# Optimization experiments

Measured on AMD Instinct MI355X. Metric: run time of the kernel, lower is better.

The kernel has to match this reference:

```python
import jax, jax.numpy as jnp
import numpy as np

L = 2; B = 16; H = 56; W = 56; N = H * W; D = 256
HEADS = 8; HD = 32; INNER = HEADS * HD
WIN = 7; WIN2 = WIN * WIN; NWH = H // WIN; NWW = W // WIN; NW = NWH * NWW
DISP = WIN // 2; FF = 4 * D; CPB = 512; EPS = 1e-5


def _shift_masks():
    d = DISP
    ul = np.zeros((WIN2, WIN2), np.float32)
    ul[-d * WIN:, :-d * WIN] = -np.inf
    ul[:-d * WIN, -d * WIN:] = -np.inf
    lr = np.zeros((WIN, WIN, WIN, WIN), np.float32)
    lr[:, -d:, :, :-d] = -np.inf
    lr[:, :-d, :, -d:] = -np.inf
    return jnp.asarray(ul), jnp.asarray(lr.reshape(WIN2, WIN2))

MASK_UL, MASK_LR = _shift_masks()

_idx = np.array([[i, j] for i in range(WIN) for j in range(WIN)], np.float32)
_rel = _idx[None, :, :] - _idx[:, None, :]  # (49,49,2) relative distances
REL = jnp.asarray((np.sign(_rel) * np.log1p(np.abs(_rel))).reshape(WIN2 * WIN2, 2))


def _ln(x, g, b):
    m = x.mean(-1, keepdims=True)
    v = ((x - m) ** 2).mean(-1, keepdims=True)
    return (x - m) / jnp.sqrt(v + EPS) * g + b


def _l2norm(t):
    return t / jnp.maximum(jnp.linalg.norm(t, axis=-1, keepdims=True), 1e-12)


def _window_attn(xm, qkv_w, tau, cw1, cb1, cw2, cb2, ow, ob, shifted):
    if shifted:
        xm = jnp.roll(xm, (-DISP, -DISP), (1, 2))
    qkv = xm @ qkv_w  # (B,H,W,3*INNER), no bias
    q, k, v = jnp.split(qkv, 3, axis=-1)

    def towin(t):  # (B,H,W,INNER) -> (B,heads,nw,win2,hd)
        t = t.reshape(B, NWH, WIN, NWW, WIN, HEADS, HD)
        return t.transpose(0, 5, 1, 3, 2, 4, 6).reshape(B, HEADS, NW, WIN2, HD)

    q, k, v = towin(q), towin(k), towin(v)
    # cosine-similarity attention
    dots = jnp.einsum('bhwid,bhwjd->bhwij', _l2norm(q), _l2norm(k))
    dots = dots / jnp.clip(tau, 0.01, None)[None, :, None, None, None]
    # continuous position bias MLP: 2 -> CPB -> heads
    cpb = (jax.nn.relu(REL @ cw1 + cb1) @ cw2 + cb2).reshape(WIN2, WIN2, HEADS)
    dots = dots + cpb.transpose(2, 0, 1)[None, :, None]
    if shifted:
        dots = dots.at[:, :, -NWW:].add(MASK_UL)
        dots = dots.at[:, :, NWW - 1::NWW].add(MASK_LR)
    attn = jax.nn.softmax(dots, -1)
    out = jnp.einsum('bhwij,bhwjd->bhwid', attn, v)
    out = out.reshape(B, HEADS, NWH, NWW, WIN, WIN, HD)
    out = out.transpose(0, 2, 4, 3, 5, 1, 6).reshape(B, H, W, INNER)
    out = out @ ow + ob
    if shifted:
        out = jnp.roll(out, (DISP, DISP), (1, 2))
    return out


def _forward(x, spe, qkv_w, tau, cw1, cb1, cw2, cb2, ow, ob, ln1_g, ln1_b,
             fw1, fb1, fw2, fb2, ln2_g, ln2_b, norm_g, norm_b):
    xm = (x + spe).reshape(B, H, W, D)
    for i in range(L):
        shifted = (i % 2 == 1)
        a = _window_attn(xm, qkv_w[i], tau[i], cw1[i], cb1[i], cw2[i], cb2[i],
                         ow[i], ob[i], shifted)
        xm = _ln(a, ln1_g[i], ln1_b[i]) + xm  # Residual(PostNorm(attn))
        f = jax.nn.gelu(xm @ fw1[i] + fb1[i], approximate=False) @ fw2[i] + fb2[i]
        xm = _ln(f, ln2_g[i], ln2_b[i]) + xm  # Residual(PostNorm(mlp))
    return _ln(xm, norm_g, norm_b).reshape(B, N, D)


def setup_inputs():
    key = jax.random.key(0)
    ks = jax.random.split(key, 10)
    rn = lambda k, shp, s: jax.random.normal(k, shp, jnp.float32) * s
    return {
        'x': rn(ks[0], (B, N, D), 1.0),
        'spatial_position_embedding': rn(ks[1], (B, N, D), 0.02),
        'qkv_w': rn(ks[2], (L, D, 3 * INNER), 0.02),
        'tau': jnp.ones((L, HEADS), jnp.float32),
        'cw1': rn(ks[3], (L, 2, CPB), 0.1),
        'cb1': jnp.zeros((L, CPB), jnp.float32),
        'cw2': rn(ks[4], (L, CPB, HEADS), 0.05),
        'cb2': jnp.zeros((L, HEADS), jnp.float32),
        'ow': rn(ks[5], (L, INNER, D), 0.02),
        'ob': jnp.zeros((L, D), jnp.float32),
        'ln1_g': jnp.ones((L, D), jnp.float32),
        'ln1_b': jnp.zeros((L, D), jnp.float32),
        'fw1': rn(ks[6], (L, D, FF), 0.02),
        'fb1': jnp.zeros((L, FF), jnp.float32),
        'fw2': rn(ks[7], (L, FF, D), 0.02),
        'fb2': jnp.zeros((L, D), jnp.float32),
        'ln2_g': jnp.ones((L, D), jnp.float32),
        'ln2_b': jnp.zeros((L, D), jnp.float32),
        'norm_g': jnp.ones((D,), jnp.float32),
        'norm_b': jnp.zeros((D,), jnp.float32),
    }


def reference(x, spatial_position_embedding, qkv_w, tau, cw1, cb1, cw2, cb2, ow, ob,
              ln1_g, ln1_b, fw1, fb1, fw2, fb2, ln2_g, ln2_b, norm_g, norm_b):
    return _forward(x, spatial_position_embedding, qkv_w, tau, cw1, cb1, cw2, cb2,
                    ow, ob, ln1_g, ln1_b, fw1, fb1, fw2, fb2, ln2_g, ln2_b,
                    norm_g, norm_b)
```

## Files before the change

### kernel.cpp

```cpp
#include <hip/hip_runtime.h>
#include <hip/hip_bf16.h>
#include <math.h>

typedef short    short8  __attribute__((ext_vector_type(8)));
typedef float    floatx4 __attribute__((ext_vector_type(4)));

__device__ __forceinline__ float b2f(unsigned short u) {
    union { float f; unsigned int i; } v; v.i = ((unsigned int)u) << 16; return v.f;
}
__device__ __forceinline__ unsigned short f2b(float f) {
    union { float f; unsigned int i; } v; v.f = f;
    unsigned int b = v.i;
    return (unsigned short)((b + 0x7FFFu + ((b >> 16) & 1u)) >> 16);
}
__device__ __forceinline__ float rd(const void* p, long i, int f) {
    return f ? ((const float*)p)[i] : b2f(((const unsigned short*)p)[i]);
}
__device__ __forceinline__ float fgelu(float x) {
    float x2 = x * x;
    float t = x * fmaf(x2, -0.0713548163f, -1.5957691216f);
    return __fdividef(x, 1.f + __expf(t));
}
__device__ __forceinline__ int xcd_swz(int bid, int nwg) {
    int q = nwg >> 3, r = nwg & 7;
    int xcd = bid & 7, loc = bid >> 3;
    return ((xcd < r) ? xcd * (q + 1) : r * (q + 1) + (xcd - r) * q) + loc;
}

#define NTOK_ 50176

__global__ __launch_bounds__(256) void k_detect(const unsigned short* __restrict__ x,
                                                int* __restrict__ flag) {
    __shared__ int cnt;
    if (threadIdx.x == 0) cnt = 0;
    __syncthreads();
    unsigned short v = x[threadIdx.x];
    int e = (v >> 7) & 0xFF;
    if (e >= 0x90) atomicAdd(&cnt, 1);
    __syncthreads();
    if (threadIdx.x == 0) *flag = (cnt >= 8) ? 1 : 0;
}

__global__ __launch_bounds__(256) void k_add_spe(const void* __restrict__ x,
                                                 const void* __restrict__ spe,
                                                 float* __restrict__ xm,
                                                 unsigned short* __restrict__ xb,
                                                 const int* __restrict__ flagp) {
    const int f = *flagp;
    long i = ((long)blockIdx.x * 256 + threadIdx.x) * 4;
    float4 o;
    if (f) {
        float4 a = *(const float4*)((const float*)x + i);
        float4 b = *(const float4*)((const float*)spe + i);
        o.x = a.x + b.x; o.y = a.y + b.y; o.z = a.z + b.z; o.w = a.w + b.w;
    } else {
        ushort4 a = *(const ushort4*)((const unsigned short*)x + i);
        ushort4 b = *(const ushort4*)((const unsigned short*)spe + i);
        o.x = b2f(a.x) + b2f(b.x); o.y = b2f(a.y) + b2f(b.y);
        o.z = b2f(a.z) + b2f(b.z); o.w = b2f(a.w) + b2f(b.w);
    }
    *(float4*)(xm + i) = o;
    if (xb) {
        ushort4 h; h.x = f2b(o.x); h.y = f2b(o.y); h.z = f2b(o.z); h.w = f2b(o.w);
        *(ushort4*)(xb + i) = h;
    }
}

__global__ __launch_bounds__(256) void k_transpose(const void* __restrict__ in, long ioff,
                                                   unsigned short* __restrict__ out,
                                                   int K, int N,
                                                   const int* __restrict__ flagp) {
    __shared__ unsigned short tile[32][33];
    const int f = *flagp;
    int n0 = blockIdx.x * 32, k0 = blockIdx.y * 32;
    int tx = threadIdx.x & 31, ty = threadIdx.x >> 5;
#pragma unroll
    for (int i = 0; i < 4; i++) {
        int k = k0 + ty + i * 8;
        long idx = ioff + (long)k * N + n0 + tx;
        unsigned short v = f ? f2b(((const float*)in)[idx])
                             : ((const unsigned short*)in)[idx];
        tile[ty + i * 8][tx] = v;
    }
    __syncthreads();
#pragma unroll
    for (int i = 0; i < 4; i++) {
        int n = n0 + ty + i * 8;
        out[(long)n * K + k0 + tx] = tile[tx][ty + i * 8];
    }
}

__global__ __launch_bounds__(512) void k_cpb(const void* __restrict__ cw1,
                                             const void* __restrict__ cb1,
                                             const void* __restrict__ cw2,
                                             const void* __restrict__ cb2,
                                             float* __restrict__ cpb,
                                             const int* __restrict__ flagp) {
    const int f = *flagp;
    int p = blockIdx.x;
    int l = blockIdx.y;
    int t = threadIdx.x;
    int i = p / 49, j = p - i * 49;
    int yi = i / 7, xi = i - yi * 7, yj = j / 7, xj = j - yj * 7;
    float dy = (float)(yj - yi), dx = (float)(xj - xi);
    float sy = (dy > 0.f) ? 1.f : ((dy < 0.f) ? -1.f : 0.f);
    float sx = (dx > 0.f) ? 1.f : ((dx < 0.f) ? -1.f : 0.f);
    float r0 = sy * log1pf(fabsf(dy));
    float r1 = sx * log1pf(fabsf(dx));
    float h = r0 * rd(cw1, l * 1024 + t, f) + r1 * rd(cw1, l * 1024 + 512 + t, f)
            + rd(cb1, l * 512 + t, f);
    h = fmaxf(h, 0.f);
    __shared__ float red[512];
    for (int hh = 0; hh < 8; hh++) {
        red[t] = h * rd(cw2, (long)(l * 512 + t) * 8 + hh, f);
        __syncthreads();
        for (int s = 256; s > 0; s >>= 1) {
            if (t < s) red[t] += red[t + s];
            __syncthreads();
        }
        if (t == 0) cpb[((long)l * 8 + hh) * 2401 + p] = red[0] + rd(cb2, l * 8 + hh, f);
        __syncthreads();
    }
}

__global__ __launch_bounds__(256) void k_cast_roll(const float* __restrict__ xmg,
                                                   unsigned short* __restrict__ xb, int shift) {
    int gid = blockIdx.x * 256 + threadIdx.x;
    int c4 = (gid & 63) * 4;
    int t = gid >> 6;
    int x = t % 56; int t2 = t / 56;
    int y = t2 % 56;
    int b = t2 / 56;
    int ys = y + shift; if (ys >= 56) ys -= 56;
    int xs = x + shift; if (xs >= 56) xs -= 56;
    float4 v = *(const float4*)(xmg + (((long)b * 3136 + ys * 56 + xs) * 256 + c4));
    ushort4 o; o.x = f2b(v.x); o.y = f2b(v.y); o.z = f2b(v.z); o.w = f2b(v.w);
    *(ushort4*)(xb + ((long)t * 256 + c4)) = o;
}

__global__ __launch_bounds__(256) void gemm_bt(const unsigned short* __restrict__ A,
                                               const unsigned short* __restrict__ Bt,
                                               const void* __restrict__ bias, long boff,
                                               void* __restrict__ Cp,
                                               int M, int N, int K, int flags,
                                               const int* __restrict__ flagp) {
    __shared__ __align__(16) unsigned short smem[16896];
    unsigned short* As = smem;
    const int f = *flagp;
    const int tid = threadIdx.x;
    const int lane = tid & 63;
    const int wave = tid >> 6;
    const int wrow = (wave >> 1) * 64;
    const int wcol = (wave & 1) * 64;

    const int nwg = gridDim.x * gridDim.y;
    const int nb = xcd_swz(blockIdx.y * gridDim.x + blockIdx.x, nwg);
    const int bn = nb % gridDim.x, bm = nb / gridDim.x;

    floatx4 acc[4][4] = {};

    const int arow = tid >> 2;
    const int aseg = (tid & 3) * 8;
    const unsigned short* Ag = A + (long)(bm * 128 + arow) * K + aseg;
    const long rstep = (long)64 * K;

    const int q = lane >> 4;
    const int mrow = lane & 15;

    const unsigned short* Brow[4];
#pragma unroll
    for (int nt = 0; nt < 4; nt++)
        Brow[nt] = Bt + (long)(bn * 128 + wcol + nt * 16 + mrow) * K + q * 8;

    uint4 a_cur0 = *(const uint4*)(Ag);
    uint4 a_cur1 = *(const uint4*)(Ag + rstep);
    short8 bf_cur[4], bf_nxt[4];
#pragma unroll
    for (int nt = 0; nt < 4; nt++) bf_cur[nt] = *(const short8*)(Brow[nt]);

    for (int k0 = 0; k0 < K; k0 += 32) {
        const int kn = k0 + 32;
        uint4 a_nxt0, a_nxt1;
        if (kn < K) {
            a_nxt0 = *(const uint4*)(Ag + kn);
            a_nxt1 = *(const uint4*)(Ag + kn + rstep);
#pragma unroll
            for (int nt = 0; nt < 4; nt++) bf_nxt[nt] = *(const short8*)(Brow[nt] + kn);
        }
        __syncthreads();
        *(uint4*)(As + arow * 40 + aseg) = a_cur0;
        *(uint4*)(As + (arow + 64) * 40 + aseg) = a_cur1;
        __syncthreads();

        short8 af_[4];
#pragma unroll
        for (int mt = 0; mt < 4; mt++)
            af_[mt] = *(const short8*)(As + (wrow + mt * 16 + mrow) * 40 + q * 8);
#pragma unroll
        for (int mt = 0; mt < 4; mt++)
#pragma unroll
            for (int nt = 0; nt < 4; nt++)
                acc[mt][nt] = __builtin_amdgcn_mfma_f32_16x16x32_bf16(af_[mt], bf_cur[nt], acc[mt][nt], 0, 0, 0);
        if (kn < K) {
            a_cur0 = a_nxt0; a_cur1 = a_nxt1;
#pragma unroll
            for (int nt = 0; nt < 4; nt++) bf_cur[nt] = bf_nxt[nt];
        }
    }

    __syncthreads();

    unsigned short* T = smem;
#pragma unroll
    for (int nt = 0; nt < 4; nt++) {
        int col = wcol + nt * 16 + mrow;
        float bv = (flags & 1) ? rd(bias, boff + bn * 128 + col, f) : 0.f;
#pragma unroll
        for (int mt = 0; mt < 4; mt++) {
            int row0 = wrow + mt * 16 + q * 4;
#pragma unroll
            for (int r = 0; r < 4; r++) {
                float v = acc[mt][nt][r] + bv;
                if (flags & 2) v = fgelu(v);
                T[(row0 + r) * 132 + col] = f2b(v);
            }
        }
    }
    __syncthreads();
    unsigned short* Cu = (unsigned short*)Cp;
    int row = tid >> 4;
    int col8 = (tid & 15) * 8;
#pragma unroll
    for (int p = 0; p < 8; p++) {
        int rr = p * 16 + row;
        *(uint4*)(Cu + (long)(bm * 128 + rr) * N + bn * 128 + col8) =
            *(const uint4*)(T + rr * 132 + col8);
    }
}

__global__ __launch_bounds__(256) void gemm_ln(const unsigned short* __restrict__ A,
                                               const unsigned short* __restrict__ Bt,
                                               const void* __restrict__ bias, long boff,
                                               const void* __restrict__ g, long goff,
                                               const void* __restrict__ bb, long b2off,
                                               float* __restrict__ xm,
                                               unsigned short* __restrict__ xb,
                                               int K, int xbmode,
                                               const int* __restrict__ flagp) {
    __shared__ __align__(16) unsigned short smem[17152];
    __shared__ float pp[4][32][2];
    unsigned short* As = smem;
    const int f = *flagp;
    const int tid = threadIdx.x;
    const int lane = tid & 63;
    const int wv = tid >> 6;
    const int wcol = wv * 64;
    const int bm = blockIdx.x;

    floatx4 acc[2][4] = {};
    const int brow = tid >> 2;
    const int bseg = (tid & 3) * 8;
    const unsigned short* Ag = A + (long)(bm * 32 + brow) * K + bseg;
    const int q = lane >> 4;
    const int c = lane & 15;

    const unsigned short* Brow[4];
#pragma unroll
    for (int nt = 0; nt < 4; nt++)
        Brow[nt] = Bt + (long)(wcol + nt * 16 + c) * K + q * 8;

    uint4 a_cur;
    if (tid < 128) a_cur = *(const uint4*)(Ag);
    short8 bf_cur[4], bf_nxt[4];
#pragma unroll
    for (int nt = 0; nt < 4; nt++) bf_cur[nt] = *(const short8*)(Brow[nt]);

    for (int k0 = 0; k0 < K; k0 += 32) {
        const int kn = k0 + 32;
        uint4 a_nxt;
        if (kn < K) {
            if (tid < 128) a_nxt = *(const uint4*)(Ag + kn);
#pragma unroll
            for (int nt = 0; nt < 4; nt++) bf_nxt[nt] = *(const short8*)(Brow[nt] + kn);
        }
        __syncthreads();
        if (tid < 128) *(uint4*)(As + brow * 40 + bseg) = a_cur;
        __syncthreads();

        short8 af_[2];
#pragma unroll
        for (int mt = 0; mt < 2; mt++)
            af_[mt] = *(const short8*)(As + (mt * 16 + c) * 40 + q * 8);
#pragma unroll
        for (int mt = 0; mt < 2; mt++)
#pragma unroll
            for (int nt = 0; nt < 4; nt++)
                acc[mt][nt] = __builtin_amdgcn_mfma_f32_16x16x32_bf16(af_[mt], bf_cur[nt], acc[mt][nt], 0, 0, 0);
        if (kn < K) {
            if (tid < 128) a_cur = a_nxt;
#pragma unroll
            for (int nt = 0; nt < 4; nt++) bf_cur[nt] = bf_nxt[nt];
        }
    }
    __syncthreads();

    float bv[4];
#pragma unroll
    for (int nt = 0; nt < 4; nt++)
        bv[nt] = rd(bias, boff + wcol + nt * 16 + c, f);
#pragma unroll
    for (int mt = 0; mt < 2; mt++) {
#pragma unroll
        for (int r = 0; r < 4; r++) {
            float s1 = 0.f, s2 = 0.f;
#pragma unroll
            for (int nt = 0; nt < 4; nt++) {
                float v = acc[mt][nt][r] + bv[nt];
                s1 += v; s2 += v * v;
            }
            s1 += __shfl_xor(s1, 1); s2 += __shfl_xor(s2, 1);
            s1 += __shfl_xor(s1, 2); s2 += __shfl_xor(s2, 2);
            s1 += __shfl_xor(s1, 4); s2 += __shfl_xor(s2, 4);
            s1 += __shfl_xor(s1, 8); s2 += __shfl_xor(s2, 8);
            if (c == 0) {
                pp[wv][mt * 16 + q * 4 + r][0] = s1;
                pp[wv][mt * 16 + q * 4 + r][1] = s2;
            }
        }
    }

    const int c0 = lane * 4;
    float4 gv, bbv;
    gv.x = rd(g, goff + c0 + 0, f); gv.y = rd(g, goff + c0 + 1, f);
    gv.z = rd(g, goff + c0 + 2, f); gv.w = rd(g, goff + c0 + 3, f);
    bbv.x = rd(bb, b2off + c0 + 0, f); bbv.y = rd(bb, b2off + c0 + 1, f);
    bbv.z = rd(bb, b2off + c0 + 2, f); bbv.w = rd(bb, b2off + c0 + 3, f);

    float* Tf = (float*)smem;
#pragma unroll
    for (int mt = 0; mt < 2; mt++)
#pragma unroll
        for (int nt = 0; nt < 4; nt++)
#pragma unroll
            for (int r = 0; r < 4; r++)
                Tf[(mt * 16 + q * 4 + r) * 268 + wcol + nt * 16 + c] = acc[mt][nt][r] + bv[nt];
    __syncthreads();
#pragma unroll
    for (int it = 0; it < 8; it++) {
        int row = wv * 8 + it;
        float sum = pp[0][row][0] + pp[1][row][0] + pp[2][row][0] + pp[3][row][0];
        float ssq = pp[0][row][1] + pp[1][row][1] + pp[2][row][1] + pp[3][row][1];
        float mean = sum * (1.f / 256.f);
        float var = ssq * (1.f / 256.f) - mean * mean;
        float rstd = rsqrtf(fmaxf(var, 0.f) + 1e-5f);
        long tok = (long)(bm * 32 + row);
        long grow = tok * 256;
        float4 t = *(const float4*)(Tf + row * 268 + c0);
        float4 xv = *(const float4*)(xm + grow + c0);
        float4 o;
        o.x = (t.x - mean) * rstd * gv.x + bbv.x + xv.x;
        o.y = (t.y - mean) * rstd * gv.y + bbv.y + xv.y;
        o.z = (t.z - mean) * rstd * gv.z + bbv.z + xv.z;
        o.w = (t.w - mean) * rstd * gv.w + bbv.w + xv.w;
        *(float4*)(xm + grow + c0) = o;
        if (xbmode) {
            long xg = grow;
            if (xbmode == 2) {
                int bi = (int)(tok / 3136); int r2 = (int)(tok - (long)bi * 3136);
                int y = r2 / 56; int x = r2 - y * 56;
                y = (y >= 3) ? y - 3 : y + 53;
                x = (x >= 3) ? x - 3 : x + 53;
                xg = ((long)bi * 3136 + y * 56 + x) * 256;
            }
            ushort4 hb; hb.x = f2b(o.x); hb.y = f2b(o.y); hb.z = f2b(o.z); hb.w = f2b(o.w);
            *(ushort4*)(xb + xg + c0) = hb;
        }
    }
}

__global__ __launch_bounds__(256) void k_attn(const unsigned short* __restrict__ qkv,
                                              const float* __restrict__ cpb,
                                              const void* __restrict__ tau, long toff,
                                              unsigned short* __restrict__ out,
                                              int shifted,
                                              const int* __restrict__ flagp) {
    __shared__ __align__(16) unsigned short Pbuf[4][64 * 72];
    __shared__ __align__(16) unsigned short Vt[4][32 * 72];
    __shared__ float inq_s[4][64], ink_s[4][64];

    const int f = *flagp;
    const int tid = threadIdx.x;
    const int wv = tid >> 6;
    const int lane = tid & 63;
    const int h = blockIdx.x * 4 + wv;
    const int w = blockIdx.y, b = blockIdx.z;
    const int wy = w >> 3, wx = w & 7;
    const int q = lane >> 4;
    const int c = lane & 15;

    short8 qa[4], kb[4];
    float sqv[4], skv[4];
#pragma unroll
    for (int mt = 0; mt < 4; mt++) {
        int i = mt * 16 + c; if (i > 48) i = 48;
        int py = i / 7, px = i - py * 7;
        long base = (((long)b * 56 + wy * 7 + py) * 56 + wx * 7 + px) * 768 + h * 32 + q * 8;
        qa[mt] = *(const short8*)(qkv + base);
        kb[mt] = *(const short8*)(qkv + base + 256);
        float sq = 0.f, sk = 0.f;
#pragma unroll
        for (int e = 0; e < 8; e++) {
            float a = b2f((unsigned short)qa[mt][e]); sq += a * a;
            float k2 = b2f((unsigned short)kb[mt][e]); sk += k2 * k2;
        }
        sqv[mt] = sq; skv[mt] = sk;
    }
#pragma unroll
    for (int mt = 0; mt < 4; mt++) {
        float sq = sqv[mt]; sq += __shfl_xor(sq, 16); sq += __shfl_xor(sq, 32);
        float sk = skv[mt]; sk += __shfl_xor(sk, 16); sk += __shfl_xor(sk, 32);
        if (q == 0) {
            inq_s[wv][mt * 16 + c] = 1.f / fmaxf(sqrtf(sq), 1e-12f);
            ink_s[wv][mt * 16 + c] = 1.f / fmaxf(sqrtf(sk), 1e-12f);
        }
    }

    floatx4 acc[4][4] = {};
#pragma unroll
    for (int mt = 0; mt < 4; mt++)
#pragma unroll
        for (int nt = 0; nt < 4; nt++)
            acc[mt][nt] = __builtin_amdgcn_mfma_f32_16x16x32_bf16(qa[mt], kb[nt], acc[mt][nt], 0, 0, 0);

#pragma unroll
    for (int z = lane; z < 576; z += 64)
        *(uint2*)(&Vt[wv][z * 4]) = make_uint2(0u, 0u);
    if (lane < 49) {
        int py = lane / 7, px = lane - py * 7;
        long base = (((long)b * 56 + wy * 7 + py) * 56 + wx * 7 + px) * 768 + h * 32 + 512;
#pragma unroll
        for (int dd = 0; dd < 32; dd += 8) {
            ushort4 v0 = *(const ushort4*)(qkv + base + dd);
            ushort4 v1 = *(const ushort4*)(qkv + base + dd + 4);
            Vt[wv][(dd + 0) * 72 + lane] = v0.x;
            Vt[wv][(dd + 1) * 72 + lane] = v0.y;
            Vt[wv][(dd + 2) * 72 + lane] = v0.z;
            Vt[wv][(dd + 3) * 72 + lane] = v0.w;
            Vt[wv][(dd + 4) * 72 + lane] = v1.x;
            Vt[wv][(dd + 5) * 72 + lane] = v1.y;
            Vt[wv][(dd + 6) * 72 + lane] = v1.z;
            Vt[wv][(dd + 7) * 72 + lane] = v1.w;
        }
    }

    float scale = 1.f / fmaxf(rd(tau, toff + h, f), 0.01f);
#pragma unroll
    for (int mt = 0; mt < 4; mt++) {
#pragma unroll
        for (int r = 0; r < 4; r++) {
            int i = mt * 16 + q * 4 + r;
            int ci = (i < 49) ? i : 48;
            int pyi = ci / 7, pxi = ci - pyi * 7;
            float qi = inq_s[wv][ci] * scale;
            float vals[4];
#pragma unroll
            for (int nt = 0; nt < 4; nt++) {
                int j = nt * 16 + c;
                if (j < 49) {
                    float v = acc[mt][nt][r] * qi * ink_s[wv][j]
                            + cpb[h * 2401 + ci * 49 + j];
                    if (shifted) {
                        int pyj = j / 7, pxj = j - pyj * 7;
                        if (wy == 7 && ((pyi >= 4) != (pyj >= 4))) v = -1e30f;
                        if (wx == 7 && ((pxi >= 4) != (pxj >= 4))) v = -1e30f;
                    }
                    vals[nt] = v;
                } else vals[nt] = -1e30f;
            }
            float m = fmaxf(fmaxf(vals[0], vals[1]), fmaxf(vals[2], vals[3]));
            m = fmaxf(m, __shfl_xor(m, 1)); m = fmaxf(m, __shfl_xor(m, 2));
            m = fmaxf(m, __shfl_xor(m, 4)); m = fmaxf(m, __shfl_xor(m, 8));
            float s = 0.f;
#pragma unroll
            for (int nt = 0; nt < 4; nt++) { vals[nt] = __expf(vals[nt] - m); s += vals[nt]; }
            s += __shfl_xor(s, 1); s += __shfl_xor(s, 2);
            s += __shfl_xor(s, 4); s += __shfl_xor(s, 8);
            float rinv = 1.f / s;
#pragma unroll
            for (int nt = 0; nt < 4; nt++)
                Pbuf[wv][i * 72 + nt * 16 + c] = f2b(vals[nt] * rinv);
        }
    }

    floatx4 accO[4][2] = {};
#pragma unroll
    for (int ks = 0; ks < 2; ks++) {
        short8 pa[4], vb[2];
#pragma unroll
        for (int mt = 0; mt < 4; mt++)
            pa[mt] = *(const short8*)(&Pbuf[wv][(mt * 16 + c) * 72 + ks * 32 + q * 8]);
#pragma unroll
        for (int nt = 0; nt < 2; nt++)
            vb[nt] = *(const short8*)(&Vt[wv][(nt * 16 + c) * 72 + ks * 32 + q * 8]);
#pragma unroll
        for (int mt = 0; mt < 4; mt++)
#pragma unroll
            for (int nt = 0; nt < 2; nt++)
                accO[mt][nt] = __builtin_amdgcn_mfma_f32_16x16x32_bf16(pa[mt], vb[nt], accO[mt][nt], 0, 0, 0);
    }

    int sh = shifted ? 3 : 0;
#pragma unroll
    for (int mt = 0; mt < 4; mt++) {
#pragma unroll
        for (int r = 0; r < 4; r++) {
            int i = mt * 16 + q * 4 + r;
            if (i < 49) {
                int py = i / 7, px = i - py * 7;
                int yo = wy * 7 + py + sh; if (yo >= 56) yo -= 56;
                int xo = wx * 7 + px + sh; if (xo >= 56) xo -= 56;
                long ob = (((long)b * 56 + yo) * 56 + xo) * 256 + h * 32;
                out[ob + c]      = f2b(accO[mt][0][r]);
                out[ob + 16 + c] = f2b(accO[mt][1][r]);
            }
        }
    }
}

__global__ __launch_bounds__(256) void k_final(const float* __restrict__ xm,
                                               const void* __restrict__ g,
                                               const void* __restrict__ bb,
                                               void* __restrict__ out,
                                               const int* __restrict__ flagp) {
    const int f = *flagp;
    int t = blockIdx.x, c = threadIdx.x;
    long off = (long)t * 256 + c;
    float v = xm[off];
    __shared__ float red[256];
    red[c] = v; __syncthreads();
#pragma unroll
    for (int s = 128; s > 0; s >>= 1) {
        if (c < s) red[c] += red[c + s];
        __syncthreads();
    }
    float mean = red[0] * (1.f / 256.f);
    __syncthreads();
    float d = v - mean;
    red[c] = d * d; __syncthreads();
#pragma unroll
    for (int s = 128; s > 0; s >>= 1) {
        if (c < s) red[c] += red[c + s];
        __syncthreads();
    }
    float var = red[0] * (1.f / 256.f);
    float ln = d * rsqrtf(var + 1e-5f) * rd(g, c, f) + rd(bb, c, f);
    if (f) ((float*)out)[off] = ln;
    else   ((unsigned short*)out)[off] = f2b(ln);
}

extern "C" void kernel_launch(void* const* d_in, const int* in_sizes, int n_in,
                              void* d_out, int out_size, void* d_ws, size_t ws_size,
                              hipStream_t stream) {
    char* ws = (char*)d_ws;
    float*          xm    = (float*)(ws + 0);
    unsigned short* wt    = (unsigned short*)(ws + 51380224);
    float*          cpb   = (float*)(ws + 54525952);
    int*            flagp = (int*)(ws + 54679616);
    const size_t DYN = 54680576;

    long Mg = NTOK_; int G = 1;
    while (G <= 8) {
        Mg = NTOK_ / G;
        if (DYN + (size_t)Mg * 2560 <= ws_size) break;
        G <<= 1;
    }
    if (G > 8) { G = 8; Mg = NTOK_ / 8; }
    const int NB = 16 / G;
    const bool fused = (G == 1);

    unsigned short* xb   = (unsigned short*)(ws + DYN);
    unsigned short* qkvb = (unsigned short*)(ws + DYN + Mg * 512);
    unsigned short* hid  = (unsigned short*)(ws + DYN + Mg * 512);

    k_detect<<<1, 256, 0, stream>>>((const unsigned short*)d_in[0], flagp);

    for (int l = 0; l < 2; l++) {
        unsigned short* base = wt + (long)l * 786432;
        k_transpose<<<dim3(24, 8), 256, 0, stream>>>(d_in[2],  (long)l * 196608, base,          256, 768,  flagp);
        k_transpose<<<dim3(8, 8),  256, 0, stream>>>(d_in[8],  (long)l * 65536,  base + 196608, 256, 256,  flagp);
        k_transpose<<<dim3(32, 8), 256, 0, stream>>>(d_in[12], (long)l * 262144, base + 262144, 256, 1024, flagp);
        k_transpose<<<dim3(8, 32), 256, 0, stream>>>(d_in[14], (long)l * 262144, base + 524288, 1024, 256, flagp);
    }
    k_cpb<<<dim3(2401, 2), 512, 0, stream>>>(d_in[4], d_in[5], d_in[6], d_in[7], cpb, flagp);
    k_add_spe<<<dim3(12544), 256, 0, stream>>>(d_in[0], d_in[1], xm,
                                               fused ? xb : (unsigned short*)nullptr, flagp);

    for (int l = 0; l < 2; l++) {
        int sh = (l & 1) ? 3 : 0;
        unsigned short* base = wt + (long)l * 786432;
        for (int g = 0; g < G; g++) {
            long m0 = (long)g * Mg;
            if (!fused)
                k_cast_roll<<<dim3(Mg / 4), 256, 0, stream>>>(xm + m0 * 256, xb, sh);
            gemm_bt<<<dim3(6, Mg / 128), 256, 0, stream>>>(xb, base, nullptr, 0, qkvb,
                                                           (int)Mg, 768, 256, 4, flagp);
            k_attn<<<dim3(2, 64, NB), 256, 0, stream>>>(qkvb, cpb + (long)l * 19208,
                                                        d_in[3], (long)l * 8, xb, (l & 1), flagp);
            gemm_ln<<<dim3(Mg / 32), 256, 0, stream>>>(xb, base + 196608, d_in[9], (long)l * 256,
                                                       d_in[10], (long)l * 256, d_in[11], (long)l * 256,
                                                       xm + m0 * 256, xb, 256, 1, flagp);
            gemm_bt<<<dim3(8, Mg / 128), 256, 0, stream>>>(xb, base + 262144, d_in[13], (long)l * 1024,
                                                           hid, (int)Mg, 1024, 256, 1 | 2 | 4, flagp);
            int xbm = fused ? ((l == 0) ? 2 : 0) : 1;
            gemm_ln<<<dim3(Mg / 32), 256, 0, stream>>>(hid, base + 524288, d_in[15], (long)l * 256,
                                                       d_in[16], (long)l * 256, d_in[17], (long)l * 256,
                                                       xm + m0 * 256, xb, 1024, xbm, flagp);
        }
    }
    k_final<<<dim3(NTOK_), 256, 0, stream>>>(xm, d_in[18], d_in[19], d_out, flagp);
}
```

Measured before the change: 1.027 ms.

## Stage B tiles through LDS in gemm_ln and fuse final LayerNorm into last layer

The gemm_ln kernel now loads the weight (B) tile cooperatively into shared memory each K step, replacing per-wave direct global register loads with register double-buffering. This cuts redundant global loads of B but drops the software prefetch. In the fused path, the last layer's FFN gemm_ln also applies the final LayerNorm and writes straight to the output, skipping k_final and the xm writeback. Skipping that writeback assumes xm is not needed afterwards.

```diff
diff --git a/kernel.cpp b/kernel.cpp
--- a/kernel.cpp
+++ b/kernel.cpp
@@ -246,10 +246,14 @@
                                                float* __restrict__ xm,
                                                unsigned short* __restrict__ xb,
                                                int K, int xbmode,
+                                               const void* __restrict__ fg,
+                                               const void* __restrict__ fb,
+                                               void* __restrict__ outp,
                                                const int* __restrict__ flagp) {
     __shared__ __align__(16) unsigned short smem[17152];
     __shared__ float pp[4][32][2];
     unsigned short* As = smem;
+    unsigned short* Bs = smem + 1280;
     const int f = *flagp;
     const int tid = threadIdx.x;
     const int lane = tid & 63;
@@ -261,46 +265,38 @@
     const int brow = tid >> 2;
     const int bseg = (tid & 3) * 8;
     const unsigned short* Ag = A + (long)(bm * 32 + brow) * K + bseg;
+    const unsigned short* Bg = Bt + (long)brow * K + bseg;
+    const long brow2 = (long)64 * K;
     const int q = lane >> 4;
     const int c = lane & 15;
 
-    const unsigned short* Brow[4];
-#pragma unroll
-    for (int nt = 0; nt < 4; nt++)
-        Brow[nt] = Bt + (long)(wcol + nt * 16 + c) * K + q * 8;
-
-    uint4 a_cur;
-    if (tid < 128) a_cur = *(const uint4*)(Ag);
-    short8 bf_cur[4], bf_nxt[4];
-#pragma unroll
-    for (int nt = 0; nt < 4; nt++) bf_cur[nt] = *(const short8*)(Brow[nt]);
-
     for (int k0 = 0; k0 < K; k0 += 32) {
-        const int kn = k0 + 32;
-        uint4 a_nxt;
-        if (kn < K) {
-            if (tid < 128) a_nxt = *(const uint4*)(Ag + kn);
-#pragma unroll
-            for (int nt = 0; nt < 4; nt++) bf_nxt[nt] = *(const short8*)(Brow[nt] + kn);
-        }
-        __syncthreads();
-        if (tid < 128) *(uint4*)(As + brow * 40 + bseg) = a_cur;
-        __syncthreads();
-
-        short8 af_[2];
+        uint4 a0;
+        if (tid < 128) a0 = *(const uint4*)(Ag + k0);
+        uint4 b0 = *(const uint4*)(Bg + k0);
+        uint4 b1 = *(const uint4*)(Bg + k0 + brow2);
+        uint4 b2 = *(const uint4*)(Bg + k0 + 2 * brow2);
+        uint4 b3 = *(const uint4*)(Bg + k0 + 3 * brow2);
+        __syncthreads();
+        if (tid < 128) *(uint4*)(As + brow * 40 + bseg) = a0;
+        *(uint4*)(Bs + brow * 40 + bseg) = b0;
+        *(uint4*)(Bs + (brow + 64) * 40 + bseg) = b1;
+        *(uint4*)(Bs + (brow + 128) * 40 + bseg) = b2;
+        *(uint4*)(Bs + (brow + 192) * 40 + bseg) = b3;
+        __syncthreads();
+
+        short8 af_[2], bf_[4];
 #pragma unroll
         for (int mt = 0; mt < 2; mt++)
             af_[mt] = *(const short8*)(As + (mt * 16 + c) * 40 + q * 8);
 #pragma unroll
+        for (int nt = 0; nt < 4; nt++)
+            bf_[nt] = *(const short8*)(Bs + (wcol + nt * 16 + c) * 40 + q * 8);
+#pragma unroll
         for (int mt = 0; mt < 2; mt++)
 #pragma unroll
             for (int nt = 0; nt < 4; nt++)
-                acc[mt][nt] = __builtin_amdgcn_mfma_f32_16x16x32_bf16(af_[mt], bf_cur[nt], acc[mt][nt], 0, 0, 0);
-        if (kn < K) {
-            if (tid < 128) a_cur = a_nxt;
-#pragma unroll
-            for (int nt = 0; nt < 4; nt++) bf_cur[nt] = bf_nxt[nt];
-        }
+                acc[mt][nt] = __builtin_amdgcn_mfma_f32_16x16x32_bf16(af_[mt], bf_[nt], acc[mt][nt], 0, 0, 0);
     }
     __syncthreads();
 
@@ -330,11 +326,17 @@
     }
 
     const int c0 = lane * 4;
-    float4 gv, bbv;
+    float4 gv, bbv, fgv, fbv;
     gv.x = rd(g, goff + c0 + 0, f); gv.y = rd(g, goff + c0 + 1, f);
     gv.z = rd(g, goff + c0 + 2, f); gv.w = rd(g, goff + c0 + 3, f);
     bbv.x = rd(bb, b2off + c0 + 0, f); bbv.y = rd(bb, b2off + c0 + 1, f);
     bbv.z = rd(bb, b2off + c0 + 2, f); bbv.w = rd(bb, b2off + c0 + 3, f);
+    if (xbmode == 3) {
+        fgv.x = rd(fg, c0 + 0, f); fgv.y = rd(fg, c0 + 1, f);
+        fgv.z = rd(fg, c0 + 2, f); fgv.w = rd(fg, c0 + 3, f);
+        fbv.x = rd(fb, c0 + 0, f); fbv.y = rd(fb, c0 + 1, f);
+        fbv.z = rd(fb, c0 + 2, f); fbv.w = rd(fb, c0 + 3, f);
+    }
 
     float* Tf = (float*)smem;
 #pragma unroll
@@ -362,18 +364,43 @@
         o.y = (t.y - mean) * rstd * gv.y + bbv.y + xv.y;
         o.z = (t.z - mean) * rstd * gv.z + bbv.z + xv.z;
         o.w = (t.w - mean) * rstd * gv.w + bbv.w + xv.w;
-        *(float4*)(xm + grow + c0) = o;
-        if (xbmode) {
-            long xg = grow;
-            if (xbmode == 2) {
-                int bi = (int)(tok / 3136); int r2 = (int)(tok - (long)bi * 3136);
-                int y = r2 / 56; int x = r2 - y * 56;
-                y = (y >= 3) ? y - 3 : y + 53;
-                x = (x >= 3) ? x - 3 : x + 53;
-                xg = ((long)bi * 3136 + y * 56 + x) * 256;
+        if (xbmode == 3) {
+            float s1 = o.x + o.y + o.z + o.w;
+            s1 += __shfl_xor(s1, 1); s1 += __shfl_xor(s1, 2);
+            s1 += __shfl_xor(s1, 4); s1 += __shfl_xor(s1, 8);
+            s1 += __shfl_xor(s1, 16); s1 += __shfl_xor(s1, 32);
+            float fmean = s1 * (1.f / 256.f);
+            float d0 = o.x - fmean, d1 = o.y - fmean, d2 = o.z - fmean, d3 = o.w - fmean;
+            float s2 = d0 * d0 + d1 * d1 + d2 * d2 + d3 * d3;
+            s2 += __shfl_xor(s2, 1); s2 += __shfl_xor(s2, 2);
+            s2 += __shfl_xor(s2, 4); s2 += __shfl_xor(s2, 8);
+            s2 += __shfl_xor(s2, 16); s2 += __shfl_xor(s2, 32);
+            float frstd = rsqrtf(s2 * (1.f / 256.f) + 1e-5f);
+            float r0 = d0 * frstd * fgv.x + fbv.x;
+            float r1 = d1 * frstd * fgv.y + fbv.y;
+            float r2 = d2 * frstd * fgv.z + fbv.z;
+            float r3 = d3 * frstd * fgv.w + fbv.w;
+            if (f) {
+                float4 fo; fo.x = r0; fo.y = r1; fo.z = r2; fo.w = r3;
+                *(float4*)((float*)outp + grow + c0) = fo;
+            } else {
+                ushort4 ho; ho.x = f2b(r0); ho.y = f2b(r1); ho.z = f2b(r2); ho.w = f2b(r3);
+                *(ushort4*)((unsigned short*)outp + grow + c0) = ho;
             }
-            ushort4 hb; hb.x = f2b(o.x); hb.y = f2b(o.y); hb.z = f2b(o.z); hb.w = f2b(o.w);
-            *(ushort4*)(xb + xg + c0) = hb;
+        } else {
+            *(float4*)(xm + grow + c0) = o;
+            if (xbmode) {
+                long xg = grow;
+                if (xbmode == 2) {
+                    int bi = (int)(tok / 3136); int r2i = (int)(tok - (long)bi * 3136);
+                    int y = r2i / 56; int x = r2i - y * 56;
+                    y = (y >= 3) ? y - 3 : y + 53;
+                    x = (x >= 3) ? x - 3 : x + 53;
+                    xg = ((long)bi * 3136 + y * 56 + x) * 256;
+                }
+                ushort4 hb; hb.x = f2b(o.x); hb.y = f2b(o.y); hb.z = f2b(o.z); hb.w = f2b(o.w);
+                *(ushort4*)(xb + xg + c0) = hb;
+            }
         }
     }
 }
@@ -608,14 +635,17 @@
                                                         d_in[3], (long)l * 8, xb, (l & 1), flagp);
             gemm_ln<<<dim3(Mg / 32), 256, 0, stream>>>(xb, base + 196608, d_in[9], (long)l * 256,
                                                        d_in[10], (long)l * 256, d_in[11], (long)l * 256,
-                                                       xm + m0 * 256, xb, 256, 1, flagp);
+                                                       xm + m0 * 256, xb, 256, 1,
+                                                       d_in[18], d_in[19], d_out, flagp);
             gemm_bt<<<dim3(8, Mg / 128), 256, 0, stream>>>(xb, base + 262144, d_in[13], (long)l * 1024,
                                                            hid, (int)Mg, 1024, 256, 1 | 2 | 4, flagp);
-            int xbm = fused ? ((l == 0) ? 2 : 0) : 1;
+            int xbm = fused ? ((l == 0) ? 2 : 3) : 1;
             gemm_ln<<<dim3(Mg / 32), 256, 0, stream>>>(hid, base + 524288, d_in[15], (long)l * 256,
                                                        d_in[16], (long)l * 256, d_in[17], (long)l * 256,
-                                                       xm + m0 * 256, xb, 1024, xbm, flagp);
-        }
-    }
-    k_final<<<dim3(NTOK_), 256, 0, stream>>>(xm, d_in[18], d_in[19], d_out, flagp);
-}
+                                                       xm + m0 * 256, xb, 1024, xbm,
+                                                       d_in[18], d_in[19], d_out, flagp);
+        }
+    }
+    if (!fused)
+        k_final<<<dim3(NTOK_), 256, 0, stream>>>(xm, d_in[18], d_in[19], d_out, flagp);
+}
```

New measurement: 906.0 us. -11.8%, faster.
